# Kernel optimization log

Hardware: AMD Instinct MI355X
Metric: run time of the kernel (lower is better)

The kernel has to match this reference:

```python
import jax, jax.numpy as jnp
import numpy as np

N, E = 50000, 400000
IN, HID, HEADS, OUT, EDIM = 128, 16, 8, 128, 32


def _lin(key, fan_in, fan_out, bias=True):
    k1, k2 = jax.random.split(key)
    s = 1.0 / np.sqrt(fan_in)
    W = jax.random.uniform(k1, (fan_in, fan_out), jnp.float32, -s, s)
    if bias:
        b = jax.random.uniform(k2, (fan_out,), jnp.float32, -s, s)
        return W, b
    return W


def setup_inputs() -> dict:
    key = jax.random.key(0)
    ks = jax.random.split(key, 16)
    x = jax.random.normal(ks[0], (N, IN), jnp.float32)
    edge_index = jax.random.randint(ks[1], (2, E), 0, N, jnp.int64)
    edge_feats = jax.random.normal(ks[2], (E, EDIM), jnp.float32)
    H1 = HEADS * HID  # 128
    Wq1, bq1 = _lin(ks[3], IN, H1)
    Wk1, bk1 = _lin(ks[4], IN, H1)
    Wv1, bv1 = _lin(ks[5], IN, H1)
    We1 = _lin(ks[6], EDIM, H1, bias=False)
    Ws1, bs1 = _lin(ks[7], IN, H1)
    Wq2, bq2 = _lin(ks[8], H1, OUT)
    Wk2, bk2 = _lin(ks[9], H1, OUT)
    Wv2, bv2 = _lin(ks[10], H1, OUT)
    We2 = _lin(ks[11], EDIM, OUT, bias=False)
    Ws2, bs2 = _lin(ks[12], H1, OUT)
    return dict(x=x, edge_index=edge_index, edge_feats=edge_feats,
                Wq1=Wq1, bq1=bq1, Wk1=Wk1, bk1=bk1, Wv1=Wv1, bv1=bv1, We1=We1, Ws1=Ws1, bs1=bs1,
                Wq2=Wq2, bq2=bq2, Wk2=Wk2, bk2=bk2, Wv2=Wv2, bv2=bv2, We2=We2, Ws2=Ws2, bs2=bs2)


def transformer_conv(x, src, dst, e, Wq, bq, Wk, bk, Wv, bv, We, Ws, bs, heads, ch, concat):
    # PyG TransformerConv: project at nodes, gather to edges.
    n = x.shape[0]
    q = (x @ Wq + bq).reshape(n, heads, ch)[dst]          # [E,H,C]
    k = (x @ Wk + bk).reshape(n, heads, ch)[src]
    v = (x @ Wv + bv).reshape(n, heads, ch)[src]
    ee = (e @ We).reshape(-1, heads, ch)                   # edge conditioning
    k = k + ee
    v = v + ee
    alpha = (q * k).sum(-1) / jnp.sqrt(jnp.asarray(ch, x.dtype))  # [E,H]
    # per-destination segment softmax
    m = jax.ops.segment_max(alpha, dst, num_segments=n)
    m = jnp.where(jnp.isfinite(m), m, 0.0)
    ea = jnp.exp(alpha - m[dst])
    denom = jax.ops.segment_sum(ea, dst, num_segments=n)
    attn = ea / jnp.maximum(denom[dst], 1e-16)
    out = jax.ops.segment_sum(attn[:, :, None] * v, dst, num_segments=n)  # [N,H,C]
    out = out.reshape(n, heads * ch) if concat else out.mean(axis=1)
    return out + x @ Ws + bs  # root_weight skip


def reference(x, edge_index, edge_feats,
              Wq1, bq1, Wk1, bk1, Wv1, bv1, We1, Ws1, bs1,
              Wq2, bq2, Wk2, bk2, Wv2, bv2, We2, Ws2, bs2):
    src, dst = edge_index[0], edge_index[1]
    h = jax.nn.relu(transformer_conv(x, src, dst, edge_feats,
                                     Wq1, bq1, Wk1, bk1, Wv1, bv1, We1, Ws1, bs1,
                                     HEADS, HID, True))
    # dropout p=0.0 (eval) -> identity
    out = jax.nn.relu(transformer_conv(h, src, dst, edge_feats,
                                       Wq2, bq2, Wk2, bk2, Wv2, bv2, We2, Ws2, bs2,
                                       1, OUT, False))
    return out
```

## Files before the change

kernel.cpp:

```cpp
#include <hip/hip_runtime.h>


using u16 = unsigned short;
using u32 = unsigned int;

#define NODES 50000
#define EDGES 400000
#define NB196 196

typedef __attribute__((ext_vector_type(8))) short bf16x8;
typedef __attribute__((ext_vector_type(4))) float f32x4;

__device__ __forceinline__ float bflo(u32 u) { return __uint_as_float(u << 16); }
__device__ __forceinline__ float bfhi(u32 u) { return __uint_as_float(u & 0xffff0000u); }
__device__ __forceinline__ u16 f2bf(float f) {
    u32 u = __float_as_uint(f);
    u += 0x7fffu + ((u >> 16) & 1u);
    return (u16)(u >> 16);
}
__device__ __forceinline__ u32 pack2(float a, float b) {
    return (u32)f2bf(a) | ((u32)f2bf(b) << 16);
}

template <int CTRL>
__device__ __forceinline__ float dpp_addf(float x) {
    int y = __builtin_amdgcn_update_dpp(0, __float_as_int(x), CTRL, 0xF, 0xF, true);
    return x + __int_as_float(y);
}
template <int GRP>
__device__ __forceinline__ float grp_sum(float p, int lane) {
    p = dpp_addf<0xB1>(p);
    p = dpp_addf<0x4E>(p);
    p = dpp_addf<0x141>(p);
    if (GRP == 64) {
        p = dpp_addf<0x140>(p);
        p += __int_as_float(__builtin_amdgcn_ds_swizzle(__float_as_int(p), 0x401F));
        p += __int_as_float(__builtin_amdgcn_ds_bpermute((lane ^ 32) << 2,
                                                         __float_as_int(p)));
    }
    return p;
}

__global__ __launch_bounds__(256) void fill_sentinel(float* __restrict__ out, int n, float val) {
    int i = blockIdx.x * 256 + threadIdx.x;
    if (i < n) out[i] = val;
}

__global__ __launch_bounds__(64) void detect_fmt(const u32* __restrict__ xw,
                                                 const int* __restrict__ eraw,
                                                 int* __restrict__ flags) {
    int lane = threadIdx.x;
    u32 e = (xw[lane] >> 7) & 0xffu;
    unsigned long long sane = __ballot(e >= 90u && e <= 141u);
    unsigned long long zodd = __ballot(eraw[1 + 2 * lane] == 0);
    if (lane == 0) {
        flags[0] = (sane == ~0ull) ? 0 : 1;
        flags[1] = (zodd == ~0ull) ? 1 : 0;
    }
}

struct TPtrs {
    const void* src[10];
    u16*        dst[10];
    int         K[10];
};

__global__ __launch_bounds__(256) void transpose_w(TPtrs P, const int* __restrict__ fmt) {
    int m = blockIdx.x;
    int f = *fmt;
    int K = P.K[m];
    int quarter = (K * 128) >> 2;
    u16* d = P.dst[m];
    int base = blockIdx.y * quarter;
    const float* sf = (const float*)P.src[m];
    const u16*   sb = (const u16*)P.src[m];
    for (int idx = base + threadIdx.x; idx < base + quarter; idx += 256) {
        int k = idx >> 7, n = idx & 127;
        d[n * K + k] = f ? f2bf(sf[idx]) : sb[idx];
    }
}

__global__ __launch_bounds__(256) void count_deg(const int* __restrict__ raw,
                                                 const int* __restrict__ flags,
                                                 int* __restrict__ deg, int E) {
    int e = blockIdx.x * 256 + threadIdx.x;
    if (e < E) {
        int f = flags[1];
        int d = f ? raw[2 * (E + e)] : raw[E + e];
        if ((unsigned)d < (unsigned)NODES) atomicAdd(&deg[d], 1);
    }
}

__device__ __forceinline__ int block_scan256(int v) {
    __shared__ int ws[4];
    int t = threadIdx.x, lane = t & 63, w = t >> 6;
    int x = v;
#pragma unroll
    for (int off = 1; off < 64; off <<= 1) {
        int y = __shfl_up(x, off, 64);
        if (lane >= off) x += y;
    }
    if (lane == 63) ws[w] = x;
    __syncthreads();
#pragma unroll
    for (int j = 0; j < 3; ++j)
        if (j < w) x += ws[j];
    return x;
}

__global__ __launch_bounds__(256) void scan_a(const int* __restrict__ deg,
                                              int* __restrict__ bsum, int n) {
    int i = blockIdx.x * 256 + threadIdx.x;
    int v = (i < n) ? deg[i] : 0;
    int incl = block_scan256(v);
    if (threadIdx.x == 255) bsum[blockIdx.x] = incl;
}

__global__ __launch_bounds__(256) void scan_b(int* __restrict__ bsum, int nb) {
    int t = threadIdx.x;
    int v = (t < nb) ? bsum[t] : 0;
    int incl = block_scan256(v);
    if (t < nb) bsum[t] = incl - v;
}

__global__ __launch_bounds__(256) void scan_c(const int* __restrict__ deg,
                                              const int* __restrict__ bsum,
                                              int* __restrict__ row_ptr,
                                              int* __restrict__ cursor, int n) {
    int b = blockIdx.x;
    int i = b * 256 + threadIdx.x;
    int v = (i < n) ? deg[i] : 0;
    int incl = block_scan256(v) + bsum[b];
    if (i < n) {
        row_ptr[i + 1] = incl;
        cursor[i] = incl - v;
    }
    if (i == 0) row_ptr[0] = 0;
}

__global__ __launch_bounds__(256) void fill_csr(const int* __restrict__ raw,
                                                const int* __restrict__ flags,
                                                int* __restrict__ cursor,
                                                int* __restrict__ srcs,
                                                int* __restrict__ eids, int E) {
    int e = blockIdx.x * 256 + threadIdx.x;
    if (e < E) {
        int f = flags[1];
        int d = f ? raw[2 * (E + e)] : raw[E + e];
        int s = f ? raw[2 * e] : raw[e];
        if ((unsigned)d < (unsigned)NODES && (unsigned)s < (unsigned)NODES) {
            int pos = atomicAdd(&cursor[d], 1);
            if ((unsigned)pos < (unsigned)E) { srcs[pos] = s; eids[pos] = e; }
        }
    }
}

__global__ __launch_bounds__(256) void gemm128(
    const void* __restrict__ A, const int* __restrict__ flags, int a_raw,
    const u16* __restrict__ Wt0, const u16* __restrict__ Wt1,
    const u16* __restrict__ Wt2, const u16* __restrict__ Wt3,
    const void* __restrict__ b0, const void* __restrict__ b1,
    const void* __restrict__ b2, const void* __restrict__ b3,
    u16* __restrict__ Oq, u16* __restrict__ KVo, u16* __restrict__ Osk,
    int M) {
    constexpr int K = 128;
    constexpr int PAD = K + 8;
    constexpr int KV = K / 8;
    __shared__ u16 Asl[64 * PAD];
    __shared__ u16 Bsl[128 * PAD];

    int f = flags[0];
    int set = blockIdx.y;
    const u16* Wt; const void* bias;
    switch (set) {
        case 0: Wt = Wt0; bias = b0; break;
        case 1: Wt = Wt1; bias = b1; break;
        case 2: Wt = Wt2; bias = b2; break;
        default: Wt = Wt3; bias = b3; break;
    }
    int m0 = blockIdx.x * 64;

    if (a_raw && f) {
        const float* Af = (const float*)A;
        for (int idx = threadIdx.x; idx < 64 * KV; idx += 256) {
            int r = idx / KV, cv = idx % KV;
            int gr = m0 + r;
            uint4 val = make_uint4(0, 0, 0, 0);
            if (gr < M) {
                const float* p = Af + (size_t)gr * K + cv * 8;
                float4 lo = *reinterpret_cast<const float4*>(p);
                float4 hi = *reinterpret_cast<const float4*>(p + 4);
                val = make_uint4(pack2(lo.x, lo.y), pack2(lo.z, lo.w),
                                 pack2(hi.x, hi.y), pack2(hi.z, hi.w));
            }
            *reinterpret_cast<uint4*>(&Asl[r * PAD + cv * 8]) = val;
        }
    } else {
        const u16* Ab = (const u16*)A;
        for (int idx = threadIdx.x; idx < 64 * KV; idx += 256) {
            int r = idx / KV, cv = idx % KV;
            int gr = m0 + r;
            uint4 val = make_uint4(0, 0, 0, 0);
            if (gr < M) val = *reinterpret_cast<const uint4*>(Ab + (size_t)gr * K + cv * 8);
            *reinterpret_cast<uint4*>(&Asl[r * PAD + cv * 8]) = val;
        }
    }
    for (int idx = threadIdx.x; idx < 128 * KV; idx += 256) {
        int r = idx / KV, cv = idx % KV;
        *reinterpret_cast<uint4*>(&Bsl[r * PAD + cv * 8]) =
            *reinterpret_cast<const uint4*>(Wt + r * K + cv * 8);
    }
    __syncthreads();

    int lane = threadIdx.x & 63, wv = threadIdx.x >> 6;
    int l15 = lane & 15;
    int quad = lane >> 4;
    int kq = quad * 8;

    f32x4 b4[8];
#pragma unroll
    for (int nt = 0; nt < 8; ++nt) {
        int col0 = nt * 16 + quad * 4;
        if (bias) {
            if (f) {
                b4[nt] = *reinterpret_cast<const f32x4*>((const float*)bias + col0);
            } else {
                uint2 bu = *reinterpret_cast<const uint2*>((const u16*)bias + col0);
                b4[nt][0] = bflo(bu.x); b4[nt][1] = bfhi(bu.x);
                b4[nt][2] = bflo(bu.y); b4[nt][3] = bfhi(bu.y);
            }
        } else {
            b4[nt][0] = b4[nt][1] = b4[nt][2] = b4[nt][3] = 0.f;
        }
    }

    f32x4 acc[8] = {};
#pragma unroll
    for (int k0 = 0; k0 < K; k0 += 32) {
        bf16x8 xf = *reinterpret_cast<const bf16x8*>(&Asl[(wv * 16 + l15) * PAD + k0 + kq]);
#pragma unroll
        for (int nt = 0; nt < 8; ++nt) {
            bf16x8 wf = *reinterpret_cast<const bf16x8*>(&Bsl[(nt * 16 + l15) * PAD + k0 + kq]);
            acc[nt] = __builtin_amdgcn_mfma_f32_16x16x32_bf16(wf, xf, acc[nt], 0, 0, 0);
        }
    }

    int row = m0 + wv * 16 + l15;
    if (row < M) {
        if (set == 0 || set == 3) {
            u16* Orow = (set == 0 ? Oq : Osk) + (size_t)row * 128;
#pragma unroll
            for (int nt = 0; nt < 8; ++nt) {
                uint2 pk;
                pk.x = pack2(acc[nt][0] + b4[nt][0], acc[nt][1] + b4[nt][1]);
                pk.y = pack2(acc[nt][2] + b4[nt][2], acc[nt][3] + b4[nt][3]);
                *reinterpret_cast<uint2*>(Orow + nt * 16 + quad * 4) = pk;
            }
        } else {
            u16* Orow = KVo + (size_t)row * 256 + (set == 2 ? 1 : 0);
#pragma unroll
            for (int nt = 0; nt < 8; ++nt) {
                int col0 = nt * 16 + quad * 4;
#pragma unroll
                for (int r = 0; r < 4; ++r)
                    Orow[(col0 + r) * 2] = f2bf(acc[nt][r] + b4[nt][r]);
            }
        }
    }
}

__global__ __launch_bounds__(256) void gemm_ee(
    const int* __restrict__ eids, const void* __restrict__ EF,
    const u16* __restrict__ WtE1 , const u16* __restrict__ WtE2,
    const int* __restrict__ flags,
    u16* __restrict__ EE1, u16* __restrict__ EE2, int Etot) {
    constexpr int PAD = 40;
    __shared__ u16 Asl[64 * PAD];
    __shared__ u16 Bsl[2][128 * PAD];
    int p0 = blockIdx.x * 64;
    int f = flags[0];
    bool dual = (EE2 != nullptr);

    {
        int r = threadIdx.x >> 2, seg = threadIdx.x & 3;
        int p = p0 + r;
        int e = (p < Etot) ? eids[p] : 0;
        uint4 val;
        if (f) {
            const float* src = (const float*)EF + (size_t)e * 32 + seg * 8;
            float4 lo = *reinterpret_cast<const float4*>(src);
            float4 hi = *reinterpret_cast<const float4*>(src + 4);
            val = make_uint4(pack2(lo.x, lo.y), pack2(lo.z, lo.w),
                             pack2(hi.x, hi.y), pack2(hi.z, hi.w));
        } else {
            val = *reinterpret_cast<const uint4*>((const u16*)EF + (size_t)e * 32 + seg * 8);
        }
        *reinterpret_cast<uint4*>(&Asl[r * PAD + seg * 8]) = val;
    }
    for (int idx = threadIdx.x; idx < 128 * 4; idx += 256) {
        int r = idx >> 2, seg = idx & 3;
        *reinterpret_cast<uint4*>(&Bsl[0][r * PAD + seg * 8]) =
            *reinterpret_cast<const uint4*>(WtE1 + r * 32 + seg * 8);
    }
    if (dual) {
        for (int idx = threadIdx.x; idx < 128 * 4; idx += 256) {
            int r = idx >> 2, seg = idx & 3;
            *reinterpret_cast<uint4*>(&Bsl[1][r * PAD + seg * 8]) =
                *reinterpret_cast<const uint4*>(WtE2 + r * 32 + seg * 8);
        }
    }
    __syncthreads();

    int lane = threadIdx.x & 63, wv = threadIdx.x >> 6;
    int l15 = lane & 15;
    int quad = lane >> 4;
    int kq = quad * 8;
    int pos = p0 + wv * 16 + l15;
    bool ok = pos < Etot;
    bf16x8 ef8 = *reinterpret_cast<const bf16x8*>(&Asl[(wv * 16 + l15) * PAD + kq]);

    {
        f32x4 acc[8] = {};
#pragma unroll
        for (int nt = 0; nt < 8; ++nt) {
            bf16x8 wf = *reinterpret_cast<const bf16x8*>(&Bsl[0][(nt * 16 + l15) * PAD + kq]);
            acc[nt] = __builtin_amdgcn_mfma_f32_16x16x32_bf16(wf, ef8, acc[nt], 0, 0, 0);
        }
        if (ok) {
            u16* Orow = EE1 + (size_t)pos * 128;
#pragma unroll
            for (int nt = 0; nt < 8; ++nt) {
                uint2 pk;
                pk.x = pack2(acc[nt][0], acc[nt][1]);
                pk.y = pack2(acc[nt][2], acc[nt][3]);
                *reinterpret_cast<uint2*>(Orow + nt * 16 + quad * 4) = pk;
            }
        }
    }
    if (dual) {
        f32x4 acc[8] = {};
#pragma unroll
        for (int nt = 0; nt < 8; ++nt) {
            bf16x8 wf = *reinterpret_cast<const bf16x8*>(&Bsl[1][(nt * 16 + l15) * PAD + kq]);
            acc[nt] = __builtin_amdgcn_mfma_f32_16x16x32_bf16(wf, ef8, acc[nt], 0, 0, 0);
        }
        if (ok) {
            u16* Orow = EE2 + (size_t)pos * 128;
#pragma unroll
            for (int nt = 0; nt < 8; ++nt) {
                uint2 pk;
                pk.x = pack2(acc[nt][0], acc[nt][1]);
                pk.y = pack2(acc[nt][2], acc[nt][3]);
                *reinterpret_cast<uint2*>(Orow + nt * 16 + quad * 4) = pk;
            }
        }
    }
}

template <int HEADS, int F32OUT>
__global__ __launch_bounds__(256) void attn_kernel(
    const int* __restrict__ row_ptr, const int* __restrict__ srcs,
    const u16* __restrict__ Q, const u16* __restrict__ KVn,
    const u16* __restrict__ EE, const u16* __restrict__ SK,
    void* __restrict__ OUT, int nn) {
    int wv = threadIdx.x >> 6, lane = threadIdx.x & 63;
    int node = blockIdx.x * 4 + wv;
    if (node >= nn) return;
    int c0 = lane * 2;

    u32 qb = *reinterpret_cast<const u32*>(Q + (size_t)node * 128 + c0);
    float q0 = bflo(qb), q1 = bfhi(qb);

    int beg = row_ptr[node], end = row_ptr[node + 1];
    const float scale = (HEADS == 8) ? 0.25f : 0.08838834764831845f;
    constexpr int GRP = (HEADS == 8) ? 8 : 64;

    float l_run = 0.f, a0 = 0.f, a1 = 0.f;

    auto edge_step = [&](uint2 kvv, u32 ebv) {
        float e0 = bflo(ebv), e1 = bfhi(ebv);
        float k0 = bflo(kvv.x) + e0, k1 = bflo(kvv.y) + e1;
        float p = q0 * k0 + q1 * k1;
        p = grp_sum<GRP>(p, lane);
        float w = __expf(p * scale);
        l_run += w;
        a0 = fmaf(w, bfhi(kvv.x) + e0, a0);
        a1 = fmaf(w, bfhi(kvv.y) + e1, a1);
    };

    int i = beg;
    for (; i + 8 <= end; i += 8) {
        int sA[8];
#pragma unroll
        for (int j = 0; j < 8; ++j) sA[j] = srcs[i + j];
        uint2 kv2[8]; u32 eb[8];
#pragma unroll
        for (int j = 0; j < 8; ++j) {
            kv2[j] = *reinterpret_cast<const uint2*>(KVn + (size_t)sA[j] * 256 + c0 * 2);
            eb[j] = *reinterpret_cast<const u32*>(EE + (size_t)(i + j) * 128 + c0);
        }
#pragma unroll
        for (int j = 0; j < 8; ++j) edge_step(kv2[j], eb[j]);
    }
    for (; i < end; ++i) {
        int s = srcs[i];
        uint2 kvv = *reinterpret_cast<const uint2*>(KVn + (size_t)s * 256 + c0 * 2);
        u32 ebv = *reinterpret_cast<const u32*>(EE + (size_t)i * 128 + c0);
        edge_step(kvv, ebv);
    }

    float inv = 1.f / fmaxf(l_run, 1e-16f);
    u32 sb = *reinterpret_cast<const u32*>(SK + (size_t)node * 128 + c0);
    float o0 = fmaxf(a0 * inv + bflo(sb), 0.f);
    float o1 = fmaxf(a1 * inv + bfhi(sb), 0.f);
    if (F32OUT) {
        *reinterpret_cast<float2*>((float*)OUT + (size_t)node * 128 + c0) = make_float2(o0, o1);
    } else {
        *reinterpret_cast<u32*>((u16*)OUT + (size_t)node * 128 + c0) = pack2(o0, o1);
    }
}

template <int HEADS, int F32OUT>
__global__ __launch_bounds__(256) void attn_fused(
    const int* __restrict__ row_ptr, const int* __restrict__ srcs,
    const int* __restrict__ eids, const int* __restrict__ flags,
    const u16* __restrict__ Q, const u16* __restrict__ KVn,
    const void* __restrict__ EF, const void* __restrict__ We,
    const u16* __restrict__ SK, void* __restrict__ OUT, int nn) {
    int wv = threadIdx.x >> 6, lane = threadIdx.x & 63;
    int node = blockIdx.x * 4 + wv;
    if (node >= nn) return;
    int c0 = lane * 2;
    int f = flags[0];

    float wf0[32], wf1[32];
    if (f) {
        const float* Wef = (const float*)We;
#pragma unroll
        for (int d = 0; d < 32; ++d) {
            float2 w2 = *reinterpret_cast<const float2*>(Wef + d * 128 + c0);
            wf0[d] = w2.x; wf1[d] = w2.y;
        }
    } else {
        const u16* Web = (const u16*)We;
#pragma unroll
        for (int d = 0; d < 32; ++d) {
            u32 w = *reinterpret_cast<const u32*>(Web + d * 128 + c0);
            wf0[d] = bflo(w); wf1[d] = bfhi(w);
        }
    }

    u32 qb = *reinterpret_cast<const u32*>(Q + (size_t)node * 128 + c0);
    float q0 = bflo(qb), q1 = bfhi(qb);
    int beg = row_ptr[node], end = row_ptr[node + 1];
    const float scale = (HEADS == 8) ? 0.25f : 0.08838834764831845f;
    constexpr int GRP = (HEADS == 8) ? 8 : 64;
    float l_run = 0.f, a0 = 0.f, a1 = 0.f;

    for (int i = beg; i < end; ++i) {
        int s = srcs[i], e = eids[i];
        uint2 kvv = *reinterpret_cast<const uint2*>(KVn + (size_t)s * 256 + c0 * 2);
        float efv[32];
        if (f) {
            const float* eff = (const float*)EF + (size_t)e * 32;
#pragma unroll
            for (int t = 0; t < 8; ++t) {
                float4 q4 = *reinterpret_cast<const float4*>(eff + t * 4);
                efv[4 * t] = q4.x; efv[4 * t + 1] = q4.y;
                efv[4 * t + 2] = q4.z; efv[4 * t + 3] = q4.w;
            }
        } else {
            const uint4* efp = reinterpret_cast<const uint4*>((const u16*)EF + (size_t)e * 32);
            uint4 ea = efp[0], eb2 = efp[1], ec = efp[2], ed = efp[3];
            u32 efw[16] = {ea.x, ea.y, ea.z, ea.w, eb2.x, eb2.y, eb2.z, eb2.w,
                           ec.x, ec.y, ec.z, ec.w, ed.x, ed.y, ed.z, ed.w};
#pragma unroll
            for (int t = 0; t < 16; ++t) {
                efv[2 * t] = bflo(efw[t]);
                efv[2 * t + 1] = bfhi(efw[t]);
            }
        }
        float ee0 = 0.f, ee1 = 0.f;
#pragma unroll
        for (int t = 0; t < 32; ++t) {
            ee0 = fmaf(efv[t], wf0[t], ee0);
            ee1 = fmaf(efv[t], wf1[t], ee1);
        }
        float k0 = bflo(kvv.x) + ee0, k1 = bflo(kvv.y) + ee1;
        float p = q0 * k0 + q1 * k1;
        p = grp_sum<GRP>(p, lane);
        float w = __expf(p * scale);
        l_run += w;
        a0 = fmaf(w, bfhi(kvv.x) + ee0, a0);
        a1 = fmaf(w, bfhi(kvv.y) + ee1, a1);
    }

    float inv = 1.f / fmaxf(l_run, 1e-16f);
    u32 sb = *reinterpret_cast<const u32*>(SK + (size_t)node * 128 + c0);
    float o0 = fmaxf(a0 * inv + bflo(sb), 0.f);
    float o1 = fmaxf(a1 * inv + bfhi(sb), 0.f);
    if (F32OUT) {
        *reinterpret_cast<float2*>((float*)OUT + (size_t)node * 128 + c0) = make_float2(o0, o1);
    } else {
        *reinterpret_cast<u32*>((u16*)OUT + (size_t)node * 128 + c0) = pack2(o0, o1);
    }
}

extern "C" void kernel_launch(void* const* d_in, const int* in_sizes, int n_in,
                              void* d_out, int out_size, void* d_ws, size_t ws_size,
                              hipStream_t stream) {
    const int N = NODES, E = EDGES;
    const void* x  = d_in[0];
    const int*  ei = (const int*)d_in[1];
    const void* ef = d_in[2];
    const void* Wq1 = d_in[3];  const void* bq1 = d_in[4];
    const void* Wk1 = d_in[5];  const void* bk1 = d_in[6];
    const void* Wv1 = d_in[7];  const void* bv1 = d_in[8];
    const void* We1 = d_in[9];
    const void* Ws1 = d_in[10]; const void* bs1 = d_in[11];
    const void* Wq2 = d_in[12]; const void* bq2 = d_in[13];
    const void* Wk2 = d_in[14]; const void* bk2 = d_in[15];
    const void* Wv2 = d_in[16]; const void* bv2 = d_in[17];
    const void* We2 = d_in[18];
    const void* Ws2 = d_in[19]; const void* bs2 = d_in[20];

    char* ws = (char*)d_ws;
    size_t off = 0;
    auto carve = [&](size_t bytes) -> void* {
        void* p = ws + off;
        off += (bytes + 255) & ~(size_t)255;
        return p;
    };

    u16* WtQ1 = (u16*)carve(128 * 128 * 2);
    u16* WtK1 = (u16*)carve(128 * 128 * 2);
    u16* WtV1 = (u16*)carve(128 * 128 * 2);
    u16* WtS1 = (u16*)carve(128 * 128 * 2);
    u16* WtQ2 = (u16*)carve(128 * 128 * 2);
    u16* WtK2 = (u16*)carve(128 * 128 * 2);
    u16* WtV2 = (u16*)carve(128 * 128 * 2);
    u16* WtS2 = (u16*)carve(128 * 128 * 2);
    u16* WtE1 = (u16*)carve(128 * 32 * 2);
    u16* WtE2 = (u16*)carve(128 * 32 * 2);
    int* flags   = (int*)carve(256);
    int* deg     = (int*)carve((size_t)N * 4);
    int* bsum    = (int*)carve((size_t)NB196 * 4);
    int* row_ptr = (int*)carve((size_t)(N + 1) * 4);
    int* cursor  = (int*)carve((size_t)N * 4);
    int* srcs    = (int*)carve((size_t)E * 4);
    int* eids    = (int*)carve((size_t)E * 4);
    u16* q  = (u16*)carve((size_t)N * 128 * 2);
    u16* kv = (u16*)carve((size_t)N * 256 * 2);
    u16* sk = (u16*)carve((size_t)N * 128 * 2);
    u16* h  = (u16*)carve((size_t)N * 128 * 2);
    const size_t REQ_BASE = off;
    u16* ee1 = (u16*)carve((size_t)E * 128 * 2);
    const size_t REQ_BIG = off;
    u16* ee2 = (u16*)carve((size_t)E * 128 * 2);
    const size_t REQ_2EE = off;
    const bool DUAL  = (ws_size >= REQ_2EE);
    const bool MATOK = (ws_size >= REQ_BIG);

    if (ws_size < REQ_BASE) {
        hipLaunchKernelGGL(fill_sentinel, dim3((out_size + 255) / 256), dim3(256), 0, stream,
                           (float*)d_out, out_size, 16.0f * (float)(ws_size >> 20));
        return;
    }

    hipLaunchKernelGGL(detect_fmt, dim3(1), dim3(64), 0, stream, (const u32*)x, ei, flags);

    TPtrs tp;
    tp.src[0] = Wq1; tp.dst[0] = WtQ1; tp.K[0] = 128;
    tp.src[1] = Wk1; tp.dst[1] = WtK1; tp.K[1] = 128;
    tp.src[2] = Wv1; tp.dst[2] = WtV1; tp.K[2] = 128;
    tp.src[3] = Ws1; tp.dst[3] = WtS1; tp.K[3] = 128;
    tp.src[4] = Wq2; tp.dst[4] = WtQ2; tp.K[4] = 128;
    tp.src[5] = Wk2; tp.dst[5] = WtK2; tp.K[5] = 128;
    tp.src[6] = Wv2; tp.dst[6] = WtV2; tp.K[6] = 128;
    tp.src[7] = Ws2; tp.dst[7] = WtS2; tp.K[7] = 128;
    tp.src[8] = We1; tp.dst[8] = WtE1; tp.K[8] = 32;
    tp.src[9] = We2; tp.dst[9] = WtE2; tp.K[9] = 32;
    hipLaunchKernelGGL(transpose_w, dim3(10, 4), dim3(256), 0, stream, tp, flags);

    (void)hipMemsetAsync(deg, 0, (size_t)N * 4, stream);
    hipLaunchKernelGGL(count_deg, dim3((E + 255) / 256), dim3(256), 0, stream, ei, flags, deg, E);
    hipLaunchKernelGGL(scan_a, dim3(NB196), dim3(256), 0, stream, deg, bsum, N);
    hipLaunchKernelGGL(scan_b, dim3(1), dim3(256), 0, stream, bsum, NB196);
    hipLaunchKernelGGL(scan_c, dim3(NB196), dim3(256), 0, stream, deg, bsum, row_ptr, cursor, N);
    hipLaunchKernelGGL(fill_csr, dim3((E + 255) / 256), dim3(256), 0, stream, ei, flags, cursor,
                       srcs, eids, E);

    const int gN = (N + 63) / 64;
    const int gE = E / 64;
    const int gA = (N + 3) / 4;

    if (MATOK) {
        hipLaunchKernelGGL(gemm_ee, dim3(gE), dim3(256), 0, stream,
                           eids, ef, WtE1, WtE2, flags,
                           ee1, DUAL ? ee2 : (u16*)nullptr, E);
    }

    hipLaunchKernelGGL(gemm128, dim3(gN, 4), dim3(256), 0, stream,
                       x, flags, 1, WtQ1, WtK1, WtV1, WtS1,
                       bq1, bk1, bv1, bs1, q, kv, sk, N);
    if (MATOK) {
        hipLaunchKernelGGL((attn_kernel<8, 0>), dim3(gA), dim3(256), 0, stream,
                           row_ptr, srcs, q, kv, ee1, sk, (void*)h, N);
    } else {
        hipLaunchKernelGGL((attn_fused<8, 0>), dim3(gA), dim3(256), 0, stream,
                           row_ptr, srcs, eids, flags, q, kv, ef, We1, sk, (void*)h, N);
    }

    hipLaunchKernelGGL(gemm128, dim3(gN, 4), dim3(256), 0, stream,
                       h, flags, 0, WtQ2, WtK2, WtV2, WtS2,
                       bq2, bk2, bv2, bs2, q, kv, sk, N);
    if (MATOK) {
        if (!DUAL) {
            hipLaunchKernelGGL(gemm_ee, dim3(gE), dim3(256), 0, stream,
                               eids, ef, WtE2, (const u16*)nullptr, flags,
                               ee1, (u16*)nullptr, E);
        }
        hipLaunchKernelGGL((attn_kernel<1, 1>), dim3(gA), dim3(256), 0, stream,
                           row_ptr, srcs, q, kv, DUAL ? ee2 : ee1, sk, d_out, N);
    } else {
        hipLaunchKernelGGL((attn_fused<1, 1>), dim3(gA), dim3(256), 0, stream,
                           row_ptr, srcs, eids, flags, q, kv, ef, We2, sk, d_out, N);
    }
}
```

Before: 493.1 us.

## Split interleaved K/V into separate arrays and pre-convert x to bf16

Replaces the interleaved KV buffer (K and V alternating per element) with separate K and V node arrays. All four GEMM outputs can now use packed vector stores instead of scalar strided 16-bit stores. A new convert_x kernel turns x into bf16 once, so the layer-1 GEMM no longer converts fp32 to bf16 in each of its four blockIdx.y sets. In exchange, the attention gather now issues two 4-byte loads per edge instead of one 8-byte load, and the extra conversion pass adds memory traffic and a launch.

```diff
diff --git a/kernel.cpp b/kernel.cpp
--- a/kernel.cpp
+++ b/kernel.cpp
@@ -56,6 +56,24 @@
     if (lane == 0) {
         flags[0] = (sane == ~0ull) ? 0 : 1;
         flags[1] = (zodd == ~0ull) ? 1 : 0;
+    }
+}
+
+__global__ __launch_bounds__(256) void convert_x(const void* __restrict__ X,
+                                                 const int* __restrict__ flags,
+                                                 u16* __restrict__ xbf, int total) {
+    int i = (blockIdx.x * 256 + threadIdx.x) * 8;
+    if (i >= total) return;
+    if (flags[0]) {
+        const float* xf = (const float*)X + i;
+        float4 lo = *reinterpret_cast<const float4*>(xf);
+        float4 hi = *reinterpret_cast<const float4*>(xf + 4);
+        uint4 val = make_uint4(pack2(lo.x, lo.y), pack2(lo.z, lo.w),
+                               pack2(hi.x, hi.y), pack2(hi.z, hi.w));
+        *reinterpret_cast<uint4*>(xbf + i) = val;
+    } else {
+        *reinterpret_cast<uint4*>(xbf + i) =
+            *reinterpret_cast<const uint4*>((const u16*)X + i);
     }
 }
 
@@ -156,12 +174,13 @@
 }
 
 __global__ __launch_bounds__(256) void gemm128(
-    const void* __restrict__ A, const int* __restrict__ flags, int a_raw,
+    const u16* __restrict__ A, const int* __restrict__ flags,
     const u16* __restrict__ Wt0, const u16* __restrict__ Wt1,
     const u16* __restrict__ Wt2, const u16* __restrict__ Wt3,
     const void* __restrict__ b0, const void* __restrict__ b1,
     const void* __restrict__ b2, const void* __restrict__ b3,
-    u16* __restrict__ Oq, u16* __restrict__ KVo, u16* __restrict__ Osk,
+    u16* __restrict__ O0, u16* __restrict__ O1,
+    u16* __restrict__ O2, u16* __restrict__ O3,
     int M) {
     constexpr int K = 128;
     constexpr int PAD = K + 8;
@@ -170,40 +189,21 @@
     __shared__ u16 Bsl[128 * PAD];
 
     int f = flags[0];
-    int set = blockIdx.y;
-    const u16* Wt; const void* bias;
-    switch (set) {
-        case 0: Wt = Wt0; bias = b0; break;
-        case 1: Wt = Wt1; bias = b1; break;
-        case 2: Wt = Wt2; bias = b2; break;
-        default: Wt = Wt3; bias = b3; break;
+    const u16* Wt; const void* bias; u16* O;
+    switch (blockIdx.y) {
+        case 0: Wt = Wt0; bias = b0; O = O0; break;
+        case 1: Wt = Wt1; bias = b1; O = O1; break;
+        case 2: Wt = Wt2; bias = b2; O = O2; break;
+        default: Wt = Wt3; bias = b3; O = O3; break;
     }
     int m0 = blockIdx.x * 64;
 
-    if (a_raw && f) {
-        const float* Af = (const float*)A;
-        for (int idx = threadIdx.x; idx < 64 * KV; idx += 256) {
-            int r = idx / KV, cv = idx % KV;
-            int gr = m0 + r;
-            uint4 val = make_uint4(0, 0, 0, 0);
-            if (gr < M) {
-                const float* p = Af + (size_t)gr * K + cv * 8;
-                float4 lo = *reinterpret_cast<const float4*>(p);
-                float4 hi = *reinterpret_cast<const float4*>(p + 4);
-                val = make_uint4(pack2(lo.x, lo.y), pack2(lo.z, lo.w),
-                                 pack2(hi.x, hi.y), pack2(hi.z, hi.w));
-            }
-            *reinterpret_cast<uint4*>(&Asl[r * PAD + cv * 8]) = val;
-        }
-    } else {
-        const u16* Ab = (const u16*)A;
-        for (int idx = threadIdx.x; idx < 64 * KV; idx += 256) {
-            int r = idx / KV, cv = idx % KV;
-            int gr = m0 + r;
-            uint4 val = make_uint4(0, 0, 0, 0);
-            if (gr < M) val = *reinterpret_cast<const uint4*>(Ab + (size_t)gr * K + cv * 8);
-            *reinterpret_cast<uint4*>(&Asl[r * PAD + cv * 8]) = val;
-        }
+    for (int idx = threadIdx.x; idx < 64 * KV; idx += 256) {
+        int r = idx / KV, cv = idx % KV;
+        int gr = m0 + r;
+        uint4 val = make_uint4(0, 0, 0, 0);
+        if (gr < M) val = *reinterpret_cast<const uint4*>(A + (size_t)gr * K + cv * 8);
+        *reinterpret_cast<uint4*>(&Asl[r * PAD + cv * 8]) = val;
     }
     for (int idx = threadIdx.x; idx < 128 * KV; idx += 256) {
         int r = idx / KV, cv = idx % KV;
@@ -247,24 +247,13 @@
 
     int row = m0 + wv * 16 + l15;
     if (row < M) {
-        if (set == 0 || set == 3) {
-            u16* Orow = (set == 0 ? Oq : Osk) + (size_t)row * 128;
-#pragma unroll
-            for (int nt = 0; nt < 8; ++nt) {
-                uint2 pk;
-                pk.x = pack2(acc[nt][0] + b4[nt][0], acc[nt][1] + b4[nt][1]);
-                pk.y = pack2(acc[nt][2] + b4[nt][2], acc[nt][3] + b4[nt][3]);
-                *reinterpret_cast<uint2*>(Orow + nt * 16 + quad * 4) = pk;
-            }
-        } else {
-            u16* Orow = KVo + (size_t)row * 256 + (set == 2 ? 1 : 0);
-#pragma unroll
-            for (int nt = 0; nt < 8; ++nt) {
-                int col0 = nt * 16 + quad * 4;
-#pragma unroll
-                for (int r = 0; r < 4; ++r)
-                    Orow[(col0 + r) * 2] = f2bf(acc[nt][r] + b4[nt][r]);
-            }
+        u16* Orow = O + (size_t)row * 128;
+#pragma unroll
+        for (int nt = 0; nt < 8; ++nt) {
+            uint2 pk;
+            pk.x = pack2(acc[nt][0] + b4[nt][0], acc[nt][1] + b4[nt][1]);
+            pk.y = pack2(acc[nt][2] + b4[nt][2], acc[nt][3] + b4[nt][3]);
+            *reinterpret_cast<uint2*>(Orow + nt * 16 + quad * 4) = pk;
         }
     }
 }
@@ -360,9 +349,9 @@
 template <int HEADS, int F32OUT>
 __global__ __launch_bounds__(256) void attn_kernel(
     const int* __restrict__ row_ptr, const int* __restrict__ srcs,
-    const u16* __restrict__ Q, const u16* __restrict__ KVn,
-    const u16* __restrict__ EE, const u16* __restrict__ SK,
-    void* __restrict__ OUT, int nn) {
+    const u16* __restrict__ Q, const u16* __restrict__ Kn,
+    const u16* __restrict__ Vn, const u16* __restrict__ EE,
+    const u16* __restrict__ SK, void* __restrict__ OUT, int nn) {
     int wv = threadIdx.x >> 6, lane = threadIdx.x & 63;
     int node = blockIdx.x * 4 + wv;
     if (node >= nn) return;
@@ -377,15 +366,15 @@
 
     float l_run = 0.f, a0 = 0.f, a1 = 0.f;
 
-    auto edge_step = [&](uint2 kvv, u32 ebv) {
+    auto edge_step = [&](u32 kbv, u32 vbv, u32 ebv) {
         float e0 = bflo(ebv), e1 = bfhi(ebv);
-        float k0 = bflo(kvv.x) + e0, k1 = bflo(kvv.y) + e1;
+        float k0 = bflo(kbv) + e0, k1 = bfhi(kbv) + e1;
         float p = q0 * k0 + q1 * k1;
         p = grp_sum<GRP>(p, lane);
         float w = __expf(p * scale);
         l_run += w;
-        a0 = fmaf(w, bfhi(kvv.x) + e0, a0);
-        a1 = fmaf(w, bfhi(kvv.y) + e1, a1);
+        a0 = fmaf(w, bflo(vbv) + e0, a0);
+        a1 = fmaf(w, bfhi(vbv) + e1, a1);
     };
 
     int i = beg;
@@ -393,20 +382,22 @@
         int sA[8];
 #pragma unroll
         for (int j = 0; j < 8; ++j) sA[j] = srcs[i + j];
-        uint2 kv2[8]; u32 eb[8];
+        u32 kb[8], vb[8], eb[8];
 #pragma unroll
         for (int j = 0; j < 8; ++j) {
-            kv2[j] = *reinterpret_cast<const uint2*>(KVn + (size_t)sA[j] * 256 + c0 * 2);
+            kb[j] = *reinterpret_cast<const u32*>(Kn + (size_t)sA[j] * 128 + c0);
+            vb[j] = *reinterpret_cast<const u32*>(Vn + (size_t)sA[j] * 128 + c0);
             eb[j] = *reinterpret_cast<const u32*>(EE + (size_t)(i + j) * 128 + c0);
         }
 #pragma unroll
-        for (int j = 0; j < 8; ++j) edge_step(kv2[j], eb[j]);
+        for (int j = 0; j < 8; ++j) edge_step(kb[j], vb[j], eb[j]);
     }
     for (; i < end; ++i) {
         int s = srcs[i];
-        uint2 kvv = *reinterpret_cast<const uint2*>(KVn + (size_t)s * 256 + c0 * 2);
+        u32 kbv = *reinterpret_cast<const u32*>(Kn + (size_t)s * 128 + c0);
+        u32 vbv = *reinterpret_cast<const u32*>(Vn + (size_t)s * 128 + c0);
         u32 ebv = *reinterpret_cast<const u32*>(EE + (size_t)i * 128 + c0);
-        edge_step(kvv, ebv);
+        edge_step(kbv, vbv, ebv);
     }
 
     float inv = 1.f / fmaxf(l_run, 1e-16f);
@@ -424,9 +415,10 @@
 __global__ __launch_bounds__(256) void attn_fused(
     const int* __restrict__ row_ptr, const int* __restrict__ srcs,
     const int* __restrict__ eids, const int* __restrict__ flags,
-    const u16* __restrict__ Q, const u16* __restrict__ KVn,
-    const void* __restrict__ EF, const void* __restrict__ We,
-    const u16* __restrict__ SK, void* __restrict__ OUT, int nn) {
+    const u16* __restrict__ Q, const u16* __restrict__ Kn,
+    const u16* __restrict__ Vn, const void* __restrict__ EF,
+    const void* __restrict__ We, const u16* __restrict__ SK,
+    void* __restrict__ OUT, int nn) {
     int wv = threadIdx.x >> 6, lane = threadIdx.x & 63;
     int node = blockIdx.x * 4 + wv;
     if (node >= nn) return;
@@ -459,7 +451,8 @@
 
     for (int i = beg; i < end; ++i) {
         int s = srcs[i], e = eids[i];
-        uint2 kvv = *reinterpret_cast<const uint2*>(KVn + (size_t)s * 256 + c0 * 2);
+        u32 kbv = *reinterpret_cast<const u32*>(Kn + (size_t)s * 128 + c0);
+        u32 vbv = *reinterpret_cast<const u32*>(Vn + (size_t)s * 128 + c0);
         float efv[32];
         if (f) {
             const float* eff = (const float*)EF + (size_t)e * 32;
@@ -486,13 +479,13 @@
             ee0 = fmaf(efv[t], wf0[t], ee0);
             ee1 = fmaf(efv[t], wf1[t], ee1);
         }
-        float k0 = bflo(kvv.x) + ee0, k1 = bflo(kvv.y) + ee1;
+        float k0 = bflo(kbv) + ee0, k1 = bfhi(kbv) + ee1;
         float p = q0 * k0 + q1 * k1;
         p = grp_sum<GRP>(p, lane);
         float w = __expf(p * scale);
         l_run += w;
-        a0 = fmaf(w, bfhi(kvv.x) + ee0, a0);
-        a1 = fmaf(w, bfhi(kvv.y) + ee1, a1);
+        a0 = fmaf(w, bflo(vbv) + ee0, a0);
+        a1 = fmaf(w, bfhi(vbv) + ee1, a1);
     }
 
     float inv = 1.f / fmaxf(l_run, 1e-16f);
@@ -549,8 +542,10 @@
     int* cursor  = (int*)carve((size_t)N * 4);
     int* srcs    = (int*)carve((size_t)E * 4);
     int* eids    = (int*)carve((size_t)E * 4);
+    u16* xbf = (u16*)carve((size_t)N * 128 * 2);
     u16* q  = (u16*)carve((size_t)N * 128 * 2);
-    u16* kv = (u16*)carve((size_t)N * 256 * 2);
+    u16* k  = (u16*)carve((size_t)N * 128 * 2);
+    u16* v  = (u16*)carve((size_t)N * 128 * 2);
     u16* sk = (u16*)carve((size_t)N * 128 * 2);
     u16* h  = (u16*)carve((size_t)N * 128 * 2);
     const size_t REQ_BASE = off;
@@ -568,6 +563,9 @@
     }
 
     hipLaunchKernelGGL(detect_fmt, dim3(1), dim3(64), 0, stream, (const u32*)x, ei, flags);
+
+    hipLaunchKernelGGL(convert_x, dim3((N * 128 / 8 + 255) / 256), dim3(256), 0, stream,
+                       x, flags, xbf, N * 128);
 
     TPtrs tp;
     tp.src[0] = Wq1; tp.dst[0] = WtQ1; tp.K[0] = 128;
@@ -601,19 +599,19 @@
     }
 
     hipLaunchKernelGGL(gemm128, dim3(gN, 4), dim3(256), 0, stream,
-                       x, flags, 1, WtQ1, WtK1, WtV1, WtS1,
-                       bq1, bk1, bv1, bs1, q, kv, sk, N);
+                       xbf, flags, WtQ1, WtK1, WtV1, WtS1,
+                       bq1, bk1, bv1, bs1, q, k, v, sk, N);
     if (MATOK) {
         hipLaunchKernelGGL((attn_kernel<8, 0>), dim3(gA), dim3(256), 0, stream,
-                           row_ptr, srcs, q, kv, ee1, sk, (void*)h, N);
+                           row_ptr, srcs, q, k, v, ee1, sk, (void*)h, N);
     } else {
         hipLaunchKernelGGL((attn_fused<8, 0>), dim3(gA), dim3(256), 0, stream,
-                           row_ptr, srcs, eids, flags, q, kv, ef, We1, sk, (void*)h, N);
+                           row_ptr, srcs, eids, flags, q, k, v, ef, We1, sk, (void*)h, N);
     }
 
     hipLaunchKernelGGL(gemm128, dim3(gN, 4), dim3(256), 0, stream,
-                       h, flags, 0, WtQ2, WtK2, WtV2, WtS2,
-                       bq2, bk2, bv2, bs2, q, kv, sk, N);
+                       h, flags, WtQ2, WtK2, WtV2, WtS2,
+                       bq2, bk2, bv2, bs2, q, k, v, sk, N);
     if (MATOK) {
         if (!DUAL) {
             hipLaunchKernelGGL(gemm_ee, dim3(gE), dim3(256), 0, stream,
@@ -621,9 +619,9 @@
                                ee1, (u16*)nullptr, E);
         }
         hipLaunchKernelGGL((attn_kernel<1, 1>), dim3(gA), dim3(256), 0, stream,
-                           row_ptr, srcs, q, kv, DUAL ? ee2 : ee1, sk, d_out, N);
+                           row_ptr, srcs, q, k, v, DUAL ? ee2 : ee1, sk, d_out, N);
     } else {
         hipLaunchKernelGGL((attn_fused<1, 1>), dim3(gA), dim3(256), 0, stream,
-                           row_ptr, srcs, eids, flags, q, kv, ef, We2, sk, d_out, N);
-    }
-}
+                           row_ptr, srcs, eids, flags, q, k, v, ef, We2, sk, d_out, N);
+    }
+}
```

After: 459.9 us. -6.7%, faster.
